# Optimization experiments

Measured on AMD Instinct MI355X. Metric: run time of the kernel, lower is better.

The kernel has to match this reference:

```python
import jax, jax.numpy as jnp
import numpy as np
from jax.scipy.special import logsumexp

N = 4096
SINKHORN_ITERS = 50
EPS = 1e-9


def setup_inputs() -> dict:
    key = jax.random.key(0)
    # Matrix param init: torch.rand(n, n) * 2 - 1
    matrix = jax.random.uniform(key, (N, N), dtype=jnp.float32) * 2.0 - 1.0
    return {"matrix": matrix}


def reference(matrix):
    # RandomMap.P() with sinkhorn=True: 50 iterations of row then column
    # logsumexp normalization in log space, then exp + clamp_min(1e-9).
    def body(i, log_p):
        log_p = log_p - logsumexp(log_p, axis=1, keepdims=True)  # row normalize
        log_p = log_p - logsumexp(log_p, axis=0, keepdims=True)  # col normalize
        return log_p

    log_p = jax.lax.fori_loop(0, SINKHORN_ITERS, body, matrix)
    return jnp.maximum(jnp.exp(log_p), EPS)
```

## Files before the change

kernel.cpp:

```cpp
#include <hip/hip_runtime.h>
#include <cstdint>
#include <cstddef>

#define NN 4096
#define ITERS 50
#define TB 256
#define TSTRIDE 264
#define NBLK 256
#define NTHR 1024

typedef _Float16 half4v __attribute__((ext_vector_type(4)));
typedef _Float16 half8v __attribute__((ext_vector_type(8)));

#define T_BYTES (TB * TSTRIDE * 2)
#define RED_FLOATS 4096
#define SMEM_BYTES (T_BYTES + RED_FLOATS * 4 + 1024 + 1024)

#define SCOPE __HIP_MEMORY_SCOPE_AGENT


__global__ void sk_flag_init(unsigned* __restrict__ flags) {
    flags[threadIdx.x] = 0u;
}

__device__ __forceinline__ float pload(const float* p) {
    return __hip_atomic_load(p, __ATOMIC_RELAXED, SCOPE);
}
__device__ __forceinline__ void pstore(float* p, float v) {
    __hip_atomic_store(p, v, __ATOMIC_RELAXED, SCOPE);
}

__global__ __launch_bounds__(NTHR) void sk_coop(const float* __restrict__ M,
                                                float* __restrict__ out,
                                                float* __restrict__ rpart,
                                                float* __restrict__ cpart,
                                                unsigned* __restrict__ flag_r,
                                                unsigned* __restrict__ flag_cT) {
    extern __shared__ char smem[];
    _Float16* T   = (_Float16*)smem;
    float*    red = (float*)(smem + T_BYTES);
    float*    rcv = red + RED_FLOATS;
    float*    rrv = rcv + 256;

    const int t  = threadIdx.x;
    const int bi = blockIdx.x >> 4;
    const int bj = blockIdx.x & 15;
    const float* Mt = M + ((size_t)bi * TB) * NN + (size_t)bj * TB;

    #pragma unroll
    for (int i = 0; i < 16; ++i) {
        int idx = t + i * NTHR;
        int r = idx >> 6, c4 = idx & 63;
        float4 m = *(const float4*)(Mt + (size_t)r * NN + c4 * 4);
        half4v h;
        h[0] = (_Float16)__expf(m.x);
        h[1] = (_Float16)__expf(m.y);
        h[2] = (_Float16)__expf(m.z);
        h[3] = (_Float16)__expf(m.w);
        *(half4v*)&T[r * TSTRIDE + c4 * 4] = h;
    }

    for (int it = 0; it < ITERS; ++it) {
        const int par = it & 1;
        float* rp = rpart + (size_t)par * (16 * NN);
        float* cp = cpart + (size_t)par * (16 * NN);

        if (it == 0) {
            if (t < TB) rcv[t] = 1.0f;
            __syncthreads();
        } else {
            if (t < 16) {
                const unsigned want = (unsigned)it;
                while (__hip_atomic_load(&flag_cT[bj * 16 + t], __ATOMIC_RELAXED,
                                         SCOPE) < want) {
                    __builtin_amdgcn_s_sleep(1);
                }
            }
            __syncthreads();
            asm volatile("" ::: "memory");
            if (t < TB) {
                const float* cprev = cpart + (size_t)((it - 1) & 1) * (16 * NN)
                                   + (size_t)bj * 16 * 256;
                float s = 0.0f;
                #pragma unroll
                for (int g = 0; g < 16; ++g) s += pload(&cprev[g * 256 + t]);
                rcv[t] = 1.0f / s;
            }
            __syncthreads();
        }

        {
            const int row = t & 255, q = t >> 8;
            const half8v* Trow = (const half8v*)&T[row * TSTRIDE + q * 64];
            const float4* rc4  = (const float4*)(rcv + q * 64);
            float s = 0.0f;
            #pragma unroll
            for (int k = 0; k < 8; ++k) {
                half8v hv = Trow[k];
                float4 c0 = rc4[2 * k];
                float4 c1 = rc4[2 * k + 1];
                s += (float)hv[0] * c0.x + (float)hv[1] * c0.y +
                     (float)hv[2] * c0.z + (float)hv[3] * c0.w +
                     (float)hv[4] * c1.x + (float)hv[5] * c1.y +
                     (float)hv[6] * c1.z + (float)hv[7] * c1.w;
            }
            red[q * 256 + row] = s;
        }
        __syncthreads();
        if (t < TB) {
            float s = red[t] + red[256 + t] + red[512 + t] + red[768 + t];
            pstore(&rp[(bi * 16 + bj) * 256 + t], s);
        }
        __syncthreads();
        if (t == 0) {
            asm volatile("s_waitcnt vmcnt(0)" ::: "memory");
            __hip_atomic_store(&flag_r[bi * 16 + bj], (unsigned)(it + 1),
                               __ATOMIC_RELAXED, SCOPE);
        }

        if (t < 16) {
            const unsigned want = (unsigned)(it + 1);
            while (__hip_atomic_load(&flag_r[bi * 16 + t], __ATOMIC_RELAXED,
                                     SCOPE) < want) {
                __builtin_amdgcn_s_sleep(1);
            }
        }
        __syncthreads();
        asm volatile("" ::: "memory");
        if (t < TB) {
            const float* rg = rp + (size_t)bi * 16 * 256;
            float s = 0.0f;
            #pragma unroll
            for (int g = 0; g < 16; ++g) s += pload(&rg[g * 256 + t]);
            rrv[t] = 1.0f / s;
        }
        __syncthreads();

        {
            const int ch = t & 31, sub = t >> 5;
            const int w = t >> 6, lane = t & 63;
            float acc[8] = {0, 0, 0, 0, 0, 0, 0, 0};
            #pragma unroll
            for (int r = 0; r < 8; ++r) {
                const int row = sub * 8 + r;
                half8v hv = *(const half8v*)&T[row * TSTRIDE + ch * 8];
                float rr = rrv[row];
                #pragma unroll
                for (int j = 0; j < 8; ++j) acc[j] += (float)hv[j] * rr;
            }
            #pragma unroll
            for (int j = 0; j < 8; ++j) acc[j] += __shfl_down(acc[j], 32);
            if (lane < 32) {
                const int rot = (lane >> 2) & 7;
                float* rd = red + w * 256 + ch * 8;
                #pragma unroll
                for (int jj = 0; jj < 8; ++jj) {
                    int j = (jj + rot) & 7;
                    rd[j] = acc[j];
                }
            }
        }
        __syncthreads();
        if (t < TB) {
            float s = 0.0f;
            #pragma unroll
            for (int w = 0; w < 16; ++w) s += red[w * 256 + t];
            pstore(&cp[(bj * 16 + bi) * 256 + t], s);
        }
        __syncthreads();
        if (t == 0) {
            asm volatile("s_waitcnt vmcnt(0)" ::: "memory");
            __hip_atomic_store(&flag_cT[bj * 16 + bi], (unsigned)(it + 1),
                               __ATOMIC_RELAXED, SCOPE);
        }
    }

    if (t < 16) {
        while (__hip_atomic_load(&flag_cT[bj * 16 + t], __ATOMIC_RELAXED,
                                 SCOPE) < (unsigned)ITERS) {
            __builtin_amdgcn_s_sleep(1);
        }
    }
    __syncthreads();
    asm volatile("" ::: "memory");
    if (t < TB) {
        const float* cl = cpart + (size_t)((ITERS - 1) & 1) * (16 * NN)
                        + (size_t)bj * 16 * 256;
        float s = 0.0f;
        #pragma unroll
        for (int g = 0; g < 16; ++g) s += pload(&cl[g * 256 + t]);
        rcv[t] = 1.0f / s;
    }
    __syncthreads();

    float* outt = out + ((size_t)bi * TB) * NN + (size_t)bj * TB;
    #pragma unroll
    for (int i = 0; i < 16; ++i) {
        int idx = t + i * NTHR;
        int r = idx >> 6, c4 = idx & 63;
        float4 m = *(const float4*)(Mt + (size_t)r * NN + c4 * 4);
        float rr = rrv[r];
        float4 c = ((const float4*)rcv)[c4];
        float4 o;
        o.x = fmaxf(__expf(m.x) * rr * c.x, 1e-9f);
        o.y = fmaxf(__expf(m.y) * rr * c.y, 1e-9f);
        o.z = fmaxf(__expf(m.z) * rr * c.z, 1e-9f);
        o.w = fmaxf(__expf(m.w) * rr * c.w, 1e-9f);
        *(float4*)(outt + (size_t)r * NN + c4 * 4) = o;
    }
}


__global__ __launch_bounds__(256) void sk_init(float* __restrict__ rc,
                                               float* __restrict__ c_sum) {
    int j = blockIdx.x * 256 + threadIdx.x;
    rc[j] = 1.0f;
    c_sum[j] = 0.0f;
}

__global__ __launch_bounds__(256) void sk_exp(const float* __restrict__ M,
                                              float* __restrict__ E) {
    size_t idx = ((size_t)blockIdx.x * 256 + threadIdx.x) * 4;
    float4 m = *(const float4*)(M + idx);
    float4 e;
    e.x = __expf(m.x); e.y = __expf(m.y); e.z = __expf(m.z); e.w = __expf(m.w);
    *(float4*)(E + idx) = e;
}

template<bool HAS_E>
__global__ __launch_bounds__(256) void sk_row(const float* __restrict__ Mat,
                                              const float* __restrict__ rc,
                                              float* __restrict__ rr) {
    const int wave = threadIdx.x >> 6;
    const int lane = threadIdx.x & 63;
    const int row  = blockIdx.x * 4 + wave;
    const float4* __restrict__ Mrow = (const float4*)(Mat + (size_t)row * NN);
    const float4* __restrict__ RC   = (const float4*)rc;
    float s = 0.0f;
    #pragma unroll 4
    for (int k = lane; k < NN / 4; k += 64) {
        float4 m = Mrow[k];
        float4 c = RC[k];
        if (!HAS_E) {
            m.x = __expf(m.x); m.y = __expf(m.y);
            m.z = __expf(m.z); m.w = __expf(m.w);
        }
        s += m.x * c.x + m.y * c.y + m.z * c.z + m.w * c.w;
    }
    #pragma unroll
    for (int off = 32; off > 0; off >>= 1) s += __shfl_down(s, off, 64);
    if (lane == 0) rr[row] = 1.0f / s;
}

template<bool HAS_E>
__global__ __launch_bounds__(256) void sk_col(const float* __restrict__ Mat,
                                              const float* __restrict__ rr,
                                              float* __restrict__ c_sum) {
    const int j  = blockIdx.x * 256 + threadIdx.x;
    const int r0 = blockIdx.y * 64;
    const float* __restrict__ rrp = rr + r0;
    const float* __restrict__ p   = Mat + (size_t)r0 * NN + j;
    float s = 0.0f;
    #pragma unroll 8
    for (int i = 0; i < 64; ++i) {
        float m = p[(size_t)i * NN];
        if (!HAS_E) m = __expf(m);
        s += m * rrp[i];
    }
    atomicAdd(&c_sum[j], s);
}

__global__ __launch_bounds__(256) void sk_recip(float* __restrict__ c_sum,
                                                float* __restrict__ rc) {
    int j = blockIdx.x * 256 + threadIdx.x;
    rc[j] = 1.0f / c_sum[j];
    c_sum[j] = 0.0f;
}

template<bool HAS_E>
__global__ __launch_bounds__(256) void sk_final(const float* __restrict__ Mat,
                                                const float* __restrict__ rr,
                                                const float* __restrict__ rc,
                                                float* __restrict__ out) {
    const int row = blockIdx.y;
    const int c4  = blockIdx.x * 256 + threadIdx.x;
    float4 m = ((const float4*)(Mat + (size_t)row * NN))[c4];
    if (!HAS_E) {
        m.x = __expf(m.x); m.y = __expf(m.y);
        m.z = __expf(m.z); m.w = __expf(m.w);
    }
    float4 c = ((const float4*)rc)[c4];
    float  r = rr[row];
    float4 o;
    o.x = fmaxf(m.x * r * c.x, 1e-9f);
    o.y = fmaxf(m.y * r * c.y, 1e-9f);
    o.z = fmaxf(m.z * r * c.z, 1e-9f);
    o.w = fmaxf(m.w * r * c.w, 1e-9f);
    ((float4*)out)[(size_t)row * (NN / 4) + c4] = o;
}

static void launch_fallback(const float* M, float* out, char* ws, size_t ws_size,
                            hipStream_t stream) {
    float* rc    = (float*)(ws);
    float* rr    = (float*)(ws + 16 * 1024);
    float* c_sum = (float*)(ws + 32 * 1024);
    float* E     = (float*)(ws + 64 * 1024);

    const size_t need_e = 64 * 1024 + (size_t)NN * NN * sizeof(float);
    const bool   has_e  = ws_size >= need_e;

    sk_init<<<NN / 256, 256, 0, stream>>>(rc, c_sum);

    const float* Mat = M;
    if (has_e) {
        sk_exp<<<(NN * (size_t)NN) / 1024, 256, 0, stream>>>(M, E);
        Mat = E;
    }

    dim3 gcol(16, 64);
    for (int it = 0; it < ITERS; ++it) {
        if (has_e) sk_row<true ><<<NN / 4, 256, 0, stream>>>(Mat, rc, rr);
        else       sk_row<false><<<NN / 4, 256, 0, stream>>>(Mat, rc, rr);
        if (has_e) sk_col<true ><<<gcol, 256, 0, stream>>>(Mat, rr, c_sum);
        else       sk_col<false><<<gcol, 256, 0, stream>>>(Mat, rr, c_sum);
        sk_recip<<<NN / 256, 256, 0, stream>>>(c_sum, rc);
    }

    dim3 gfin(4, NN);
    if (has_e) sk_final<true ><<<gfin, 256, 0, stream>>>(Mat, rr, rc, out);
    else       sk_final<false><<<gfin, 256, 0, stream>>>(Mat, rr, rc, out);
}

extern "C" void kernel_launch(void* const* d_in, const int* in_sizes, int n_in,
                              void* d_out, int out_size, void* d_ws, size_t ws_size,
                              hipStream_t stream) {
    const float* M   = (const float*)d_in[0];
    float*       out = (float*)d_out;
    char*        ws  = (char*)d_ws;

    unsigned* flag_r  = (unsigned*)ws;
    unsigned* flag_cT = (unsigned*)(ws + 1024);
    float*    rpart   = (float*)(ws + 4096);
    float*    cpart   = (float*)(ws + 4096 + 2 * 16 * NN * sizeof(float));
    const size_t ws_need = 4096 + 4 * 16 * NN * sizeof(float);

    int dev = 0;
    (void)hipGetDevice(&dev);
    int coop = 0;
    (void)hipDeviceGetAttribute(&coop, hipDeviceAttributeCooperativeLaunch, dev);
    hipError_t eattr = hipFuncSetAttribute(
        (const void*)sk_coop, hipFuncAttributeMaxDynamicSharedMemorySize, SMEM_BYTES);

    bool done = false;
    if (coop && eattr == hipSuccess && ws_size >= ws_need) {
        sk_flag_init<<<1, 512, 0, stream>>>(flag_r);
        void* args[6] = {(void*)&M, (void*)&out, (void*)&rpart, (void*)&cpart,
                         (void*)&flag_r, (void*)&flag_cT};
        hipError_t e = hipLaunchCooperativeKernel((void*)sk_coop, dim3(NBLK),
                                                  dim3(NTHR), args, SMEM_BYTES,
                                                  stream);
        done = (e == hipSuccess);
    }
    if (!done) launch_fallback(M, out, ws, ws_size, stream);
}
```

Measured before the change: 522.4 us.

## Replace flag-based partial-sum exchange with packed 64-bit atomic fixed-point accumulators

Per-block row and column partial sums are now combined with 64-bit atomic fetch-adds. Each add carries a fixed-point value in the low 52 bits and a contributor count in the high bits, so a reader polls one word until the count reaches 16 instead of waiting on separate flags and then reading 16 partials. The buffers rotate over four slots and are re-zeroed in advance. This drops several block-wide barriers and extra global reads per iteration, but it adds atomic contention and relies on fixed-point precision and on the sums staying in range.

```diff
diff --git a/kernel.cpp b/kernel.cpp
--- a/kernel.cpp
+++ b/kernel.cpp
@@ -19,23 +19,35 @@
 #define SCOPE __HIP_MEMORY_SCOPE_AGENT
 
 
-__global__ void sk_flag_init(unsigned* __restrict__ flags) {
-    flags[threadIdx.x] = 0u;
-}
-
-__device__ __forceinline__ float pload(const float* p) {
-    return __hip_atomic_load(p, __ATOMIC_RELAXED, SCOPE);
-}
-__device__ __forceinline__ void pstore(float* p, float v) {
-    __hip_atomic_store(p, v, __ATOMIC_RELAXED, SCOPE);
+#define CNT_ONE (1ull << 52)
+#define VAL_MASK (CNT_ONE - 1ull)
+
+__global__ void sk_zero(unsigned long long* __restrict__ b) {
+    size_t i = (size_t)blockIdx.x * blockDim.x + threadIdx.x;
+    __hip_atomic_store(&b[i], 0ull, __ATOMIC_RELAXED, SCOPE);
+}
+
+__device__ __forceinline__ unsigned long long poll16(const unsigned long long* p) {
+    unsigned long long v = __hip_atomic_load(p, __ATOMIC_RELAXED, SCOPE);
+    while ((v >> 52) < 16ull) {
+        __builtin_amdgcn_s_sleep(1);
+        v = __hip_atomic_load(p, __ATOMIC_RELAXED, SCOPE);
+    }
+    return v;
+}
+
+__device__ __forceinline__ float unpack_recip(unsigned long long v) {
+    return 1.0f / ((float)(v & VAL_MASK) * 0x1p-32f);
+}
+
+__device__ __forceinline__ unsigned long long packp(float s) {
+    return CNT_ONE | (unsigned long long)(s * 4294967296.0f);
 }
 
 __global__ __launch_bounds__(NTHR) void sk_coop(const float* __restrict__ M,
                                                 float* __restrict__ out,
-                                                float* __restrict__ rpart,
-                                                float* __restrict__ cpart,
-                                                unsigned* __restrict__ flag_r,
-                                                unsigned* __restrict__ flag_cT) {
+                                                unsigned long long* __restrict__ rbuf,
+                                                unsigned long long* __restrict__ cbuf) {
     extern __shared__ char smem[];
     _Float16* T   = (_Float16*)smem;
     float*    red = (float*)(smem + T_BYTES);
@@ -61,30 +73,24 @@
     }
 
     for (int it = 0; it < ITERS; ++it) {
-        const int par = it & 1;
-        float* rp = rpart + (size_t)par * (16 * NN);
-        float* cp = cpart + (size_t)par * (16 * NN);
+        unsigned long long* rb = rbuf + (size_t)(it & 3) * NN;
+        unsigned long long* cb = cbuf + (size_t)(it & 3) * NN;
 
         if (it == 0) {
-            if (t < TB) rcv[t] = 1.0f;
+            if (t < TB) {
+                rcv[t] = 1.0f;
+                __hip_atomic_store(&cbuf[(size_t)1 * NN + (size_t)bj * TB + t],
+                                   0ull, __ATOMIC_RELAXED, SCOPE);
+            }
             __syncthreads();
         } else {
-            if (t < 16) {
-                const unsigned want = (unsigned)it;
-                while (__hip_atomic_load(&flag_cT[bj * 16 + t], __ATOMIC_RELAXED,
-                                         SCOPE) < want) {
-                    __builtin_amdgcn_s_sleep(1);
-                }
-            }
-            __syncthreads();
-            asm volatile("" ::: "memory");
             if (t < TB) {
-                const float* cprev = cpart + (size_t)((it - 1) & 1) * (16 * NN)
-                                   + (size_t)bj * 16 * 256;
-                float s = 0.0f;
-                #pragma unroll
-                for (int g = 0; g < 16; ++g) s += pload(&cprev[g * 256 + t]);
-                rcv[t] = 1.0f / s;
+                unsigned long long v = poll16(
+                    &cbuf[(size_t)((it - 1) & 3) * NN + (size_t)bj * TB + t]);
+                rcv[t] = unpack_recip(v);
+                __hip_atomic_store(&cbuf[(size_t)((it + 1) & 3) * NN
+                                         + (size_t)bj * TB + t],
+                                   0ull, __ATOMIC_RELAXED, SCOPE);
             }
             __syncthreads();
         }
@@ -107,32 +113,18 @@
             red[q * 256 + row] = s;
         }
         __syncthreads();
+
         if (t < TB) {
             float s = red[t] + red[256 + t] + red[512 + t] + red[768 + t];
-            pstore(&rp[(bi * 16 + bj) * 256 + t], s);
-        }
-        __syncthreads();
-        if (t == 0) {
+            unsigned long long pk = packp(s);
             asm volatile("s_waitcnt vmcnt(0)" ::: "memory");
-            __hip_atomic_store(&flag_r[bi * 16 + bj], (unsigned)(it + 1),
-                               __ATOMIC_RELAXED, SCOPE);
-        }
-
-        if (t < 16) {
-            const unsigned want = (unsigned)(it + 1);
-            while (__hip_atomic_load(&flag_r[bi * 16 + t], __ATOMIC_RELAXED,
-                                     SCOPE) < want) {
-                __builtin_amdgcn_s_sleep(1);
-            }
-        }
-        __syncthreads();
-        asm volatile("" ::: "memory");
-        if (t < TB) {
-            const float* rg = rp + (size_t)bi * 16 * 256;
-            float s = 0.0f;
-            #pragma unroll
-            for (int g = 0; g < 16; ++g) s += pload(&rg[g * 256 + t]);
-            rrv[t] = 1.0f / s;
+            unsigned long long* p = &rb[(size_t)bi * TB + t];
+            __hip_atomic_fetch_add(p, pk, __ATOMIC_RELAXED, SCOPE);
+            unsigned long long v = poll16(p);
+            rrv[t] = unpack_recip(v);
+            __hip_atomic_store(&rbuf[(size_t)((it + 2) & 3) * NN
+                                     + (size_t)bi * TB + t],
+                               0ull, __ATOMIC_RELAXED, SCOPE);
         }
         __syncthreads();
 
@@ -161,35 +153,22 @@
             }
         }
         __syncthreads();
+
         if (t < TB) {
             float s = 0.0f;
             #pragma unroll
             for (int w = 0; w < 16; ++w) s += red[w * 256 + t];
-            pstore(&cp[(bj * 16 + bi) * 256 + t], s);
-        }
-        __syncthreads();
-        if (t == 0) {
+            unsigned long long pk = packp(s);
             asm volatile("s_waitcnt vmcnt(0)" ::: "memory");
-            __hip_atomic_store(&flag_cT[bj * 16 + bi], (unsigned)(it + 1),
-                               __ATOMIC_RELAXED, SCOPE);
-        }
-    }
-
-    if (t < 16) {
-        while (__hip_atomic_load(&flag_cT[bj * 16 + t], __ATOMIC_RELAXED,
-                                 SCOPE) < (unsigned)ITERS) {
-            __builtin_amdgcn_s_sleep(1);
-        }
-    }
-    __syncthreads();
-    asm volatile("" ::: "memory");
+            __hip_atomic_fetch_add(&cb[(size_t)bj * TB + t], pk,
+                                   __ATOMIC_RELAXED, SCOPE);
+        }
+    }
+
     if (t < TB) {
-        const float* cl = cpart + (size_t)((ITERS - 1) & 1) * (16 * NN)
-                        + (size_t)bj * 16 * 256;
-        float s = 0.0f;
-        #pragma unroll
-        for (int g = 0; g < 16; ++g) s += pload(&cl[g * 256 + t]);
-        rcv[t] = 1.0f / s;
+        unsigned long long v = poll16(
+            &cbuf[(size_t)((ITERS - 1) & 3) * NN + (size_t)bj * TB + t]);
+        rcv[t] = unpack_recip(v);
     }
     __syncthreads();
 
@@ -338,11 +317,9 @@
     float*       out = (float*)d_out;
     char*        ws  = (char*)d_ws;
 
-    unsigned* flag_r  = (unsigned*)ws;
-    unsigned* flag_cT = (unsigned*)(ws + 1024);
-    float*    rpart   = (float*)(ws + 4096);
-    float*    cpart   = (float*)(ws + 4096 + 2 * 16 * NN * sizeof(float));
-    const size_t ws_need = 4096 + 4 * 16 * NN * sizeof(float);
+    unsigned long long* rbuf = (unsigned long long*)ws;
+    unsigned long long* cbuf = rbuf + 4 * NN;
+    const size_t ws_need = (size_t)8 * NN * sizeof(unsigned long long);
 
     int dev = 0;
     (void)hipGetDevice(&dev);
@@ -353,9 +330,8 @@
 
     bool done = false;
     if (coop && eattr == hipSuccess && ws_size >= ws_need) {
-        sk_flag_init<<<1, 512, 0, stream>>>(flag_r);
-        void* args[6] = {(void*)&M, (void*)&out, (void*)&rpart, (void*)&cpart,
-                         (void*)&flag_r, (void*)&flag_cT};
+        sk_zero<<<16, 512, 0, stream>>>(rbuf);
+        void* args[4] = {(void*)&M, (void*)&out, (void*)&rbuf, (void*)&cbuf};
         hipError_t e = hipLaunchCooperativeKernel((void*)sk_coop, dim3(NBLK),
                                                   dim3(NTHR), args, SMEM_BYTES,
                                                   stream);
```

After: 605.9 us. +16.0%, slower.
